# Kernel tuning notes

Hardware: AMD Instinct MI355X
Metric: run time of the kernel (lower is better)

Reference implementation:

```python
import jax, jax.numpy as jnp
import numpy as np

HEAD_SIZE = 64


def setup_inputs() -> dict:
    key = jax.random.key(0)
    ks = jax.random.split(key, 4)
    B, S, H, D = 8, 4096, 768, HEAD_SIZE
    scale = 1.0 / np.sqrt(H)
    return {
        "x": jax.random.normal(ks[0], (B, S, H), dtype=jnp.float32),
        "Wq": jax.random.normal(ks[1], (H, D), dtype=jnp.float32) * scale,
        "bq": jnp.zeros((D,), dtype=jnp.float32),
        "Wk": jax.random.normal(ks[2], (H, D), dtype=jnp.float32) * scale,
        "bk": jnp.zeros((D,), dtype=jnp.float32),
        "Wv": jax.random.normal(ks[3], (H, D), dtype=jnp.float32) * scale,
        "bv": jnp.zeros((D,), dtype=jnp.float32),
    }


def reference(x, Wq, bq, Wk, bk, Wv, bv):
    # x: [B, S, H]
    B, S, H = x.shape
    D = Wq.shape[1]
    q = x @ Wq + bq  # [B, S, D]
    k = x @ Wk + bk
    v = x @ Wv + bv
    # naive full score matrix [B, S, S]
    scores = jnp.einsum("bsd,btd->bst", q, k)
    causal = jnp.tril(jnp.ones((S, S), dtype=bool))  # lower-triangular mask
    scores = jnp.where(causal[None, :, :], scores, -jnp.inf)
    attn = jax.nn.softmax(scores / jnp.sqrt(jnp.float32(D)), axis=-1)
    # dropout is identity in eval/deterministic reference
    out = jnp.einsum("bst,btd->bsd", attn, v)  # [B, S, D]
    return out
```

## Files before the change

### kernel.cpp

```cpp
#include <hip/hip_runtime.h>

typedef unsigned short u16;
typedef __bf16 bf16_t;
typedef bf16_t bf16x8 __attribute__((ext_vector_type(8)));
typedef float f32x4 __attribute__((ext_vector_type(4)));
typedef u16 u16x8 __attribute__((ext_vector_type(8)));
typedef u16 u16x4 __attribute__((ext_vector_type(4)));
typedef unsigned u32x4 __attribute__((ext_vector_type(4)));

#define B_ 8
#define S_ 4096
#define H_ 768
#define M_ (B_ * S_)

__device__ __forceinline__ u16 f2b(float f) {
  unsigned u = __float_as_uint(f);
  u += 0x7fffu + ((u >> 16) & 1u);
  return (u16)(u >> 16);
}

__device__ __forceinline__ void gl_lds16(const void* g, void* l) {
  __builtin_amdgcn_global_load_lds(
      (const __attribute__((address_space(1))) void*)g,
      (__attribute__((address_space(3))) void*)l, 16, 0, 0);
}

__global__ __launch_bounds__(256) void wconv_k(const float* __restrict__ Wq,
                                               const float* __restrict__ Wk,
                                               const float* __restrict__ Wv,
                                               u16* __restrict__ WbT) {
  __shared__ float wt[64 * 68];
  const int tid = threadIdx.x;
  int mat = blockIdx.x / 12;
  int k0 = (blockIdx.x % 12) * 64;
  const float* W = (mat == 0) ? Wq : ((mat == 1) ? Wk : Wv);
  int r = tid >> 2, c0 = (tid & 3) * 16;
  const float* src = W + (size_t)(k0 + r) * 64 + c0;
#pragma unroll
  for (int j = 0; j < 16; j += 4)
    *(float4*)&wt[r * 68 + c0 + j] = *(const float4*)(src + j);
  __syncthreads();
  int d = tid >> 2;
  u16* dst = WbT + (size_t)(mat * 64 + d) * 768 + k0 + c0;
  u16x8 o0, o1;
#pragma unroll
  for (int j = 0; j < 8; ++j) o0[j] = f2b(wt[(c0 + j) * 68 + d]);
#pragma unroll
  for (int j = 0; j < 8; ++j) o1[j] = f2b(wt[(c0 + 8 + j) * 68 + d]);
  *(u16x8*)dst = o0;
  *(u16x8*)(dst + 8) = o1;
}

__global__ __launch_bounds__(256) void qkv_k(const float* __restrict__ x,
                                             const u16* __restrict__ WbT,
                                             const float* __restrict__ bq,
                                             const float* __restrict__ bk,
                                             const float* __restrict__ bv,
                                             u16* __restrict__ qb,
                                             u16* __restrict__ kb,
                                             u16* __restrict__ vbT) {
  __shared__ __align__(16) u16 smem[2 * 2560 + 2 * 7680];
  const int tid = threadIdx.x;
  const int w = tid >> 6, ln = tid & 15, qd = (tid >> 4) & 3;
  const int row0 = blockIdx.x * 64;

  const f32x4 z4 = {0.f, 0.f, 0.f, 0.f};
  f32x4 acc[4][3];
#pragma unroll
  for (int rt = 0; rt < 4; ++rt)
#pragma unroll
    for (int ct = 0; ct < 3; ++ct) acc[rt][ct] = z4;

  const int xr = tid >> 2, xc = (tid & 3) * 8;
  float4 xf0, xf1;
  u16x8 wf[3];

  auto load_t = [&](int kt) {
    const float* sx = x + (size_t)(row0 + xr) * 768 + kt * 32 + xc;
    xf0 = *(const float4*)sx;
    xf1 = *(const float4*)(sx + 4);
#pragma unroll
    for (int i = 0; i < 3; ++i) {
      int c = i * 256 + tid;
      int r = c >> 2, off = (c & 3) * 8;
      wf[i] = *(const u16x8*)(WbT + (size_t)r * 768 + kt * 32 + off);
    }
  };

  load_t(0);
  for (int kt = 0; kt < 24; ++kt) {
    u16* xs = smem + (kt & 1) * 2560;
    u16* wsb = smem + 5120 + (kt & 1) * 7680;
    {
      u16x8 v;
      v[0] = f2b(xf0.x); v[1] = f2b(xf0.y); v[2] = f2b(xf0.z); v[3] = f2b(xf0.w);
      v[4] = f2b(xf1.x); v[5] = f2b(xf1.y); v[6] = f2b(xf1.z); v[7] = f2b(xf1.w);
      *(u16x8*)&xs[xr * 40 + xc] = v;
#pragma unroll
      for (int i = 0; i < 3; ++i) {
        int c = i * 256 + tid;
        int r = c >> 2, off = (c & 3) * 8;
        *(u16x8*)&wsb[r * 40 + off] = wf[i];
      }
    }
    if (kt < 23) load_t(kt + 1);
    __syncthreads();
    bf16x8 af[4], bfr[3];
#pragma unroll
    for (int rt = 0; rt < 4; ++rt)
      af[rt] = *(const bf16x8*)&xs[(rt * 16 + ln) * 40 + qd * 8];
#pragma unroll
    for (int ct = 0; ct < 3; ++ct)
      bfr[ct] = *(const bf16x8*)&wsb[(w * 48 + ct * 16 + ln) * 40 + qd * 8];
#pragma unroll
    for (int rt = 0; rt < 4; ++rt)
#pragma unroll
      for (int ct = 0; ct < 3; ++ct)
        acc[rt][ct] = __builtin_amdgcn_mfma_f32_16x16x32_bf16(
            af[rt], bfr[ct], acc[rt][ct], 0, 0, 0);
  }
  __syncthreads();

  u16* vt = smem;
#pragma unroll
  for (int ct = 0; ct < 3; ++ct) {
    int col = w * 48 + ct * 16 + ln;
    int mat = col >> 6, d = col & 63;
    if (mat < 2) {
      const float* bp = (mat == 0) ? bq : bk;
      u16* op = (mat == 0) ? qb : kb;
      float bias = bp[d];
      float scale = (mat == 0) ? 0.18033688011112042f : 1.0f;
#pragma unroll
      for (int rt = 0; rt < 4; ++rt)
#pragma unroll
        for (int r = 0; r < 4; ++r)
          op[(size_t)(row0 + rt * 16 + qd * 4 + r) * 64 + d] =
              f2b((acc[rt][ct][r] + bias) * scale);
    } else {
      float bias = bv[d];
#pragma unroll
      for (int rt = 0; rt < 4; ++rt)
#pragma unroll
        for (int r = 0; r < 4; ++r)
          vt[d * 72 + rt * 16 + qd * 4 + r] = f2b(acc[rt][ct][r] + bias);
    }
  }
  __syncthreads();
  {
    int d = tid >> 2, so = (tid & 3) * 16;
    int b = row0 >> 12, s0 = row0 & 4095;
    u16* dst = vbT + ((size_t)b * 64 + d) * 4096 + s0;
#pragma unroll
    for (int g = 0; g < 4; ++g) {
      int ts = so + g * 4;
      int tn = (ts & 0x23) | ((ts & 4) << 2) | ((ts & 0x18) >> 1);
      *(u16x4*)(dst + ts) = *(const u16x4*)&vt[d * 72 + tn];
    }
  }
}

__global__ __launch_bounds__(256) void attn_k(const u16* __restrict__ qb,
                                              const u16* __restrict__ kb,
                                              const u16* __restrict__ vbT,
                                              float* __restrict__ po,
                                              float* __restrict__ pl) {
  __shared__ __align__(16) u16 ks[2][4096];
  __shared__ __align__(16) u16 vs[2][4096];
  const int tid = threadIdx.x;
  const int wv = tid >> 6, ln = tid & 15, qd = (tid >> 4) & 3;
  const int id = blockIdx.x;
  const int b = id & 7;
  const int j = id >> 3;
  int qi = 31, acc = 0;
  for (;;) {
    int ncq = (2 * qi + 9) >> 3;
    if (acc + ncq <= j) { acc += ncq; --qi; } else break;
  }
  const int c = j - acc;
  const int ntiles = 2 * qi + 2;
  const int nc = (2 * qi + 9) >> 3;
  const int bas = ntiles / nc, rem = ntiles % nc;
  const int tstart = c * bas + (c < rem ? c : rem);
  const int tcount = bas + (c < rem ? 1 : 0);
  const int q0 = qi * 128;
  const int q0w = q0 + wv * 32;
  const int base = b * S_;
  const u16* kg = kb + (size_t)base * 64;
  const u16* vg = vbT + (size_t)b * 64 * 4096;

  bf16x8 qf[2][2];
#pragma unroll
  for (int qt = 0; qt < 2; ++qt) {
    const u16* qrow = qb + (size_t)(base + q0w + qt * 16 + ln) * 64;
    qf[qt][0] = *(const bf16x8*)(qrow + qd * 8);
    qf[qt][1] = *(const bf16x8*)(qrow + 32 + qd * 8);
  }
  const f32x4 z4 = {0.f, 0.f, 0.f, 0.f};
  f32x4 o0[4] = {z4, z4, z4, z4};
  f32x4 o1[4] = {z4, z4, z4, z4};
  float lq0 = 0.f, lq1 = 0.f;
  const int lr = (tid & 63) >> 3, csl = tid & 7;

  auto prefetch = [&](int bufi, int tile) {
    const u16* kt_ = kg + (size_t)tile * 4096;
    const u16* vt_ = vg + tile * 64;
#pragma unroll
    for (int i = 0; i < 2; ++i) {
      int r0 = wv * 16 + i * 8;
      int r = r0 + lr;
      int cc = csl ^ (r & 7);
      gl_lds16(kt_ + r * 64 + cc * 8, &ks[bufi][r0 * 64]);
      gl_lds16(vt_ + (size_t)r * 4096 + cc * 8, &vs[bufi][r0 * 64]);
    }
  };

  prefetch(0, tstart);
  int cur = 0;
  for (int it = 0; it < tcount; ++it) {
    asm volatile("s_waitcnt vmcnt(0)" ::: "memory");
    __builtin_amdgcn_s_barrier();
    if (it + 1 < tcount) prefetch(cur ^ 1, tstart + it + 1);
    const int t0a = (tstart + it) * 64;

    if (t0a <= q0w + 31) {
      f32x4 s0[4] = {z4, z4, z4, z4};
      f32x4 s1[4] = {z4, z4, z4, z4};
      __builtin_amdgcn_s_setprio(1);
#pragma unroll
      for (int kc = 0; kc < 2; ++kc) {
        int cs = (kc * 4 + qd) ^ (ln & 7);
#pragma unroll
        for (int nt = 0; nt < 4; ++nt) {
          bf16x8 kf = *(const bf16x8*)&ks[cur][(nt * 16 + ln) * 64 + cs * 8];
          s0[nt] = __builtin_amdgcn_mfma_f32_16x16x32_bf16(kf, qf[0][kc], s0[nt], 0, 0, 0);
          s1[nt] = __builtin_amdgcn_mfma_f32_16x16x32_bf16(kf, qf[1][kc], s1[nt], 0, 0, 0);
        }
      }
      __builtin_amdgcn_s_setprio(0);
      if (t0a + 63 > q0w) {
#pragma unroll
        for (int nt = 0; nt < 4; ++nt) {
          int tg = t0a + nt * 16 + qd * 4;
#pragma unroll
          for (int r = 0; r < 4; ++r) {
            if (tg + r > q0w + ln) s0[nt][r] = -INFINITY;
            if (tg + r > q0w + 16 + ln) s1[nt][r] = -INFINITY;
          }
        }
      }
      float p0[4][4], p1[4][4];
#pragma unroll
      for (int nt = 0; nt < 4; ++nt)
#pragma unroll
        for (int r = 0; r < 4; ++r) {
          p0[nt][r] = __builtin_amdgcn_exp2f(s0[nt][r]);
          p1[nt][r] = __builtin_amdgcn_exp2f(s1[nt][r]);
          lq0 += p0[nt][r];
          lq1 += p1[nt][r];
        }
      unsigned pk0[8], pk1[8];
#pragma unroll
      for (int i = 0; i < 8; ++i) {
        int nt = i >> 1, rb = (i & 1) * 2;
        asm("v_cvt_pk_bf16_f32 %0, %1, %2"
            : "=v"(pk0[i]) : "v"(p0[nt][rb]), "v"(p0[nt][rb + 1]));
        asm("v_cvt_pk_bf16_f32 %0, %1, %2"
            : "=v"(pk1[i]) : "v"(p1[nt][rb]), "v"(p1[nt][rb + 1]));
      }
      __builtin_amdgcn_s_setprio(1);
#pragma unroll
      for (int kc = 0; kc < 2; ++kc) {
        u32x4 w0 = {pk0[4 * kc], pk0[4 * kc + 1], pk0[4 * kc + 2], pk0[4 * kc + 3]};
        u32x4 w1 = {pk1[4 * kc], pk1[4 * kc + 1], pk1[4 * kc + 2], pk1[4 * kc + 3]};
        bf16x8 a0 = __builtin_bit_cast(bf16x8, w0);
        bf16x8 a1 = __builtin_bit_cast(bf16x8, w1);
        int cs = (kc * 4 + qd) ^ (ln & 7);
#pragma unroll
        for (int nt = 0; nt < 4; ++nt) {
          bf16x8 vf = *(const bf16x8*)&vs[cur][(nt * 16 + ln) * 64 + cs * 8];
          o0[nt] = __builtin_amdgcn_mfma_f32_16x16x32_bf16(a0, vf, o0[nt], 0, 0, 0);
          o1[nt] = __builtin_amdgcn_mfma_f32_16x16x32_bf16(a1, vf, o1[nt], 0, 0, 0);
        }
      }
      __builtin_amdgcn_s_setprio(0);
    }
    cur ^= 1;
  }

  lq0 += __shfl_xor(lq0, 16);
  lq0 += __shfl_xor(lq0, 32);
  lq1 += __shfl_xor(lq1, 16);
  lq1 += __shfl_xor(lq1, 32);

  float* op = po + (size_t)c * 2097152;
  float* lpt = pl + (size_t)c * 32768;
#pragma unroll
  for (int r = 0; r < 4; ++r) {
    int row0 = base + q0w + qd * 4 + r;
    int row1 = row0 + 16;
#pragma unroll
    for (int nt = 0; nt < 4; ++nt) {
      op[(size_t)row0 * 64 + nt * 16 + ln] = o0[nt][r];
      op[(size_t)row1 * 64 + nt * 16 + ln] = o1[nt][r];
    }
  }
  if (qd == 0) {
    lpt[base + q0w + ln] = lq0;
    lpt[base + q0w + 16 + ln] = lq1;
  }
}

__global__ __launch_bounds__(256) void comb_k(const float* __restrict__ po,
                                              const float* __restrict__ pl,
                                              float* __restrict__ out) {
  int idx = blockIdx.x * 256 + threadIdx.x;
  int r = idx >> 4, d0 = (idx & 15) * 4;
  int qi = (r & 4095) >> 7;
  int nc = (2 * qi + 9) >> 3;
  const float* p = po + (size_t)r * 64 + d0;
  float4 a = *(const float4*)p;
  float l = pl[r];
  for (int cc = 1; cc < nc; ++cc) {
    float4 t = *(const float4*)(p + (size_t)cc * 2097152);
    a.x += t.x; a.y += t.y; a.z += t.z; a.w += t.w;
    l += pl[r + cc * 32768];
  }
  float inv = 1.0f / l;
  a.x *= inv; a.y *= inv; a.z *= inv; a.w *= inv;
  *(float4*)(out + (size_t)r * 64 + d0) = a;
}

extern "C" void kernel_launch(void* const* d_in, const int* in_sizes, int n_in,
                              void* d_out, int out_size, void* d_ws, size_t ws_size,
                              hipStream_t stream) {
  const float* x  = (const float*)d_in[0];
  const float* Wq = (const float*)d_in[1];
  const float* bq = (const float*)d_in[2];
  const float* Wk = (const float*)d_in[3];
  const float* bk = (const float*)d_in[4];
  const float* Wv = (const float*)d_in[5];
  const float* bv = (const float*)d_in[6];
  float* out = (float*)d_out;

  char* wsp = (char*)d_ws;
  u16* WbT = (u16*)wsp;
  u16* qb  = (u16*)(wsp + 294912);
  u16* kb  = (u16*)(wsp + 4489216);
  u16* vbT = (u16*)(wsp + 8683520);
  float* po = (float*)(wsp + 12877824);
  float* pl = (float*)(wsp + 79986688);

  hipLaunchKernelGGL(wconv_k, dim3(36), dim3(256), 0, stream, Wq, Wk, Wv, WbT);
  hipLaunchKernelGGL(qkv_k, dim3(512), dim3(256), 0, stream,
                     x, WbT, bq, bk, bv, qb, kb, vbT);
  hipLaunchKernelGGL(attn_k, dim3(1152), dim3(256), 0, stream,
                     qb, kb, vbT, po, pl);
  hipLaunchKernelGGL(comb_k, dim3(2048), dim3(256), 0, stream,
                     po, pl, out);
}
```

Baseline: 212.2 us.

## Fuse split-K combine into attention kernel via atomic last-block reduction

```diff
diff --git a/kernel.cpp b/kernel.cpp
--- a/kernel.cpp
+++ b/kernel.cpp
@@ -28,9 +28,11 @@
 __global__ __launch_bounds__(256) void wconv_k(const float* __restrict__ Wq,
                                                const float* __restrict__ Wk,
                                                const float* __restrict__ Wv,
-                                               u16* __restrict__ WbT) {
+                                               u16* __restrict__ WbT,
+                                               int* __restrict__ cnt) {
   __shared__ float wt[64 * 68];
   const int tid = threadIdx.x;
+  if (blockIdx.x == 0) cnt[tid] = 0;
   int mat = blockIdx.x / 12;
   int k0 = (blockIdx.x % 12) * 64;
   const float* W = (mat == 0) ? Wq : ((mat == 1) ? Wk : Wv);
@@ -164,7 +166,9 @@
                                               const u16* __restrict__ kb,
                                               const u16* __restrict__ vbT,
                                               float* __restrict__ po,
-                                              float* __restrict__ pl) {
+                                              float* __restrict__ pl,
+                                              int* __restrict__ cnt,
+                                              float* __restrict__ out) {
   __shared__ __align__(16) u16 ks[2][4096];
   __shared__ __align__(16) u16 vs[2][4096];
   const int tid = threadIdx.x;
@@ -293,6 +297,27 @@
   lq1 += __shfl_xor(lq1, 16);
   lq1 += __shfl_xor(lq1, 32);
 
+  if (nc == 1) {
+    float li0[4], li1[4];
+#pragma unroll
+    for (int r = 0; r < 4; ++r) {
+      li0[r] = __shfl(lq0, qd * 4 + r);
+      li1[r] = __shfl(lq1, qd * 4 + r);
+    }
+#pragma unroll
+    for (int r = 0; r < 4; ++r) {
+      int row0 = base + q0w + qd * 4 + r;
+      int row1 = row0 + 16;
+      float i0 = 1.0f / li0[r], i1 = 1.0f / li1[r];
+#pragma unroll
+      for (int nt = 0; nt < 4; ++nt) {
+        out[(size_t)row0 * 64 + nt * 16 + ln] = o0[nt][r] * i0;
+        out[(size_t)row1 * 64 + nt * 16 + ln] = o1[nt][r] * i1;
+      }
+    }
+    return;
+  }
+
   float* op = po + (size_t)c * 2097152;
   float* lpt = pl + (size_t)c * 32768;
 #pragma unroll
@@ -309,26 +334,35 @@
     lpt[base + q0w + ln] = lq0;
     lpt[base + q0w + 16 + ln] = lq1;
   }
-}
-
-__global__ __launch_bounds__(256) void comb_k(const float* __restrict__ po,
-                                              const float* __restrict__ pl,
-                                              float* __restrict__ out) {
-  int idx = blockIdx.x * 256 + threadIdx.x;
-  int r = idx >> 4, d0 = (idx & 15) * 4;
-  int qi = (r & 4095) >> 7;
-  int nc = (2 * qi + 9) >> 3;
-  const float* p = po + (size_t)r * 64 + d0;
-  float4 a = *(const float4*)p;
-  float l = pl[r];
-  for (int cc = 1; cc < nc; ++cc) {
-    float4 t = *(const float4*)(p + (size_t)cc * 2097152);
-    a.x += t.x; a.y += t.y; a.z += t.z; a.w += t.w;
-    l += pl[r + cc * 32768];
-  }
-  float inv = 1.0f / l;
-  a.x *= inv; a.y *= inv; a.z *= inv; a.w *= inv;
-  *(float4*)(out + (size_t)r * 64 + d0) = a;
+
+  __threadfence();
+  __syncthreads();
+  volatile int* flag = (volatile int*)&ks[0][0];
+  if (tid == 0) {
+    int old = atomicAdd(&cnt[(qi << 3) | b], 1);
+    *flag = old;
+  }
+  __syncthreads();
+  if (*flag == nc - 1) {
+    __threadfence();
+    const size_t rbase = (size_t)(base + q0) * 64;
+#pragma unroll
+    for (int e = 0; e < 8; ++e) {
+      int fi = tid * 8 + e;
+      int row = fi >> 4, c4 = (fi & 15) * 4;
+      size_t off = rbase + (size_t)row * 64 + c4;
+      float4 a = *(const float4*)(po + off);
+      float l = pl[base + q0 + row];
+      for (int cc = 1; cc < nc; ++cc) {
+        float4 t = *(const float4*)(po + (size_t)cc * 2097152 + off);
+        a.x += t.x; a.y += t.y; a.z += t.z; a.w += t.w;
+        l += pl[(size_t)cc * 32768 + base + q0 + row];
+      }
+      float inv = 1.0f / l;
+      a.x *= inv; a.y *= inv; a.z *= inv; a.w *= inv;
+      *(float4*)(out + off) = a;
+    }
+  }
 }
 
 extern "C" void kernel_launch(void* const* d_in, const int* in_sizes, int n_in,
@@ -350,12 +384,12 @@
   u16* vbT = (u16*)(wsp + 8683520);
   float* po = (float*)(wsp + 12877824);
   float* pl = (float*)(wsp + 79986688);
-
-  hipLaunchKernelGGL(wconv_k, dim3(36), dim3(256), 0, stream, Wq, Wk, Wv, WbT);
+  int* cnt  = (int*)(wsp + 81035264);
+
+  hipLaunchKernelGGL(wconv_k, dim3(36), dim3(256), 0, stream,
+                     Wq, Wk, Wv, WbT, cnt);
   hipLaunchKernelGGL(qkv_k, dim3(512), dim3(256), 0, stream,
                      x, WbT, bq, bk, bv, qb, kb, vbT);
   hipLaunchKernelGGL(attn_k, dim3(1152), dim3(256), 0, stream,
-                     qb, kb, vbT, po, pl);
-  hipLaunchKernelGGL(comb_k, dim3(2048), dim3(256), 0, stream,
-                     po, pl, out);
-}
+                     qb, kb, vbT, po, pl, cnt, out);
+}
```

Result: slower. 420.4 us (+98.1%).

## Double QKV projection row tile to share weight tiles across eight waves

Applied to the files above, without the earlier changes.

```diff
diff --git a/kernel.cpp b/kernel.cpp
--- a/kernel.cpp
+++ b/kernel.cpp
@@ -51,7 +51,7 @@
   *(u16x8*)(dst + 8) = o1;
 }
 
-__global__ __launch_bounds__(256) void qkv_k(const float* __restrict__ x,
+__global__ __launch_bounds__(512) void qkv_k(const float* __restrict__ x,
                                              const u16* __restrict__ WbT,
                                              const float* __restrict__ bq,
                                              const float* __restrict__ bk,
@@ -59,10 +59,12 @@
                                              u16* __restrict__ qb,
                                              u16* __restrict__ kb,
                                              u16* __restrict__ vbT) {
-  __shared__ __align__(16) u16 smem[2 * 2560 + 2 * 7680];
+  __shared__ __align__(16) u16 smem[2 * 5120 + 2 * 7680];
   const int tid = threadIdx.x;
   const int w = tid >> 6, ln = tid & 15, qd = (tid >> 4) & 3;
-  const int row0 = blockIdx.x * 64;
+  const int rh = w >> 2;
+  const int wc = w & 3;
+  const int row0 = blockIdx.x * 128;
 
   const f32x4 z4 = {0.f, 0.f, 0.f, 0.f};
   f32x4 acc[4][3];
@@ -73,34 +75,40 @@
 
   const int xr = tid >> 2, xc = (tid & 3) * 8;
   float4 xf0, xf1;
-  u16x8 wf[3];
+  u16x8 wf0, wf1;
 
   auto load_t = [&](int kt) {
     const float* sx = x + (size_t)(row0 + xr) * 768 + kt * 32 + xc;
     xf0 = *(const float4*)sx;
     xf1 = *(const float4*)(sx + 4);
-#pragma unroll
-    for (int i = 0; i < 3; ++i) {
-      int c = i * 256 + tid;
+    {
+      int r = tid >> 2, off = (tid & 3) * 8;
+      wf0 = *(const u16x8*)(WbT + (size_t)r * 768 + kt * 32 + off);
+    }
+    if (tid < 256) {
+      int c = 512 + tid;
       int r = c >> 2, off = (c & 3) * 8;
-      wf[i] = *(const u16x8*)(WbT + (size_t)r * 768 + kt * 32 + off);
+      wf1 = *(const u16x8*)(WbT + (size_t)r * 768 + kt * 32 + off);
     }
   };
 
   load_t(0);
   for (int kt = 0; kt < 24; ++kt) {
-    u16* xs = smem + (kt & 1) * 2560;
-    u16* wsb = smem + 5120 + (kt & 1) * 7680;
+    u16* xs = smem + (kt & 1) * 5120;
+    u16* wsb = smem + 10240 + (kt & 1) * 7680;
     {
       u16x8 v;
       v[0] = f2b(xf0.x); v[1] = f2b(xf0.y); v[2] = f2b(xf0.z); v[3] = f2b(xf0.w);
       v[4] = f2b(xf1.x); v[5] = f2b(xf1.y); v[6] = f2b(xf1.z); v[7] = f2b(xf1.w);
       *(u16x8*)&xs[xr * 40 + xc] = v;
-#pragma unroll
-      for (int i = 0; i < 3; ++i) {
-        int c = i * 256 + tid;
+      {
+        int r = tid >> 2, off = (tid & 3) * 8;
+        *(u16x8*)&wsb[r * 40 + off] = wf0;
+      }
+      if (tid < 256) {
+        int c = 512 + tid;
         int r = c >> 2, off = (c & 3) * 8;
-        *(u16x8*)&wsb[r * 40 + off] = wf[i];
+        *(u16x8*)&wsb[r * 40 + off] = wf1;
       }
     }
     if (kt < 23) load_t(kt + 1);
@@ -108,10 +116,10 @@
     bf16x8 af[4], bfr[3];
 #pragma unroll
     for (int rt = 0; rt < 4; ++rt)
-      af[rt] = *(const bf16x8*)&xs[(rt * 16 + ln) * 40 + qd * 8];
+      af[rt] = *(const bf16x8*)&xs[(rh * 64 + rt * 16 + ln) * 40 + qd * 8];
 #pragma unroll
     for (int ct = 0; ct < 3; ++ct)
-      bfr[ct] = *(const bf16x8*)&wsb[(w * 48 + ct * 16 + ln) * 40 + qd * 8];
+      bfr[ct] = *(const bf16x8*)&wsb[(wc * 48 + ct * 16 + ln) * 40 + qd * 8];
 #pragma unroll
     for (int rt = 0; rt < 4; ++rt)
 #pragma unroll
@@ -124,7 +132,7 @@
   u16* vt = smem;
 #pragma unroll
   for (int ct = 0; ct < 3; ++ct) {
-    int col = w * 48 + ct * 16 + ln;
+    int col = wc * 48 + ct * 16 + ln;
     int mat = col >> 6, d = col & 63;
     if (mat < 2) {
       const float* bp = (mat == 0) ? bq : bk;
@@ -135,7 +143,7 @@
       for (int rt = 0; rt < 4; ++rt)
 #pragma unroll
         for (int r = 0; r < 4; ++r)
-          op[(size_t)(row0 + rt * 16 + qd * 4 + r) * 64 + d] =
+          op[(size_t)(row0 + rh * 64 + rt * 16 + qd * 4 + r) * 64 + d] =
               f2b((acc[rt][ct][r] + bias) * scale);
     } else {
       float bias = bv[d];
@@ -143,19 +151,20 @@
       for (int rt = 0; rt < 4; ++rt)
 #pragma unroll
         for (int r = 0; r < 4; ++r)
-          vt[d * 72 + rt * 16 + qd * 4 + r] = f2b(acc[rt][ct][r] + bias);
+          vt[d * 136 + rh * 64 + rt * 16 + qd * 4 + r] =
+              f2b(acc[rt][ct][r] + bias);
     }
   }
   __syncthreads();
   {
-    int d = tid >> 2, so = (tid & 3) * 16;
+    int d = tid >> 3, so = (tid & 7) * 16;
     int b = row0 >> 12, s0 = row0 & 4095;
     u16* dst = vbT + ((size_t)b * 64 + d) * 4096 + s0;
 #pragma unroll
     for (int g = 0; g < 4; ++g) {
       int ts = so + g * 4;
-      int tn = (ts & 0x23) | ((ts & 4) << 2) | ((ts & 0x18) >> 1);
-      *(u16x4*)(dst + ts) = *(const u16x4*)&vt[d * 72 + tn];
+      int tn = (ts & 0x40) | (ts & 0x23) | ((ts & 4) << 2) | ((ts & 0x18) >> 1);
+      *(u16x4*)(dst + ts) = *(const u16x4*)&vt[d * 136 + tn];
     }
   }
 }
@@ -352,7 +361,7 @@
   float* pl = (float*)(wsp + 79986688);
 
   hipLaunchKernelGGL(wconv_k, dim3(36), dim3(256), 0, stream, Wq, Wk, Wv, WbT);
-  hipLaunchKernelGGL(qkv_k, dim3(512), dim3(256), 0, stream,
+  hipLaunchKernelGGL(qkv_k, dim3(256), dim3(512), 0, stream,
                      x, WbT, bq, bk, bv, qb, kb, vbT);
   hipLaunchKernelGGL(attn_k, dim3(1152), dim3(256), 0, stream,
                      qb, kb, vbT, po, pl);
```

Result: faster. 208.0 us, median of 2 (-2.0%).
